# Optimization experiments

Hardware: AMD Instinct MI355X
Metric: run time of the kernel (lower is better)

## Reference

```python
import jax, jax.numpy as jnp
import numpy as np

EMBED, H1, H2, IMG, MID, VOCAB = 1024, 1024, 1024, 2048, 512, 32000
N_REGIONS = 576


def lstm_cell(x, h, c, W_ih, W_hh, b_ih, b_hh):
    # PyTorch LSTM gate order: i, f, g, o
    g = x @ W_ih.T + b_ih + h @ W_hh.T + b_hh
    i, f, gg, o = jnp.split(g, 4, axis=-1)
    i, f, o = jax.nn.sigmoid(i), jax.nn.sigmoid(f), jax.nn.sigmoid(o)
    c_new = f * c + i * jnp.tanh(gg)
    h_new = o * jnp.tanh(c_new)
    return h_new, c_new


def setup_inputs() -> dict:
    key = jax.random.key(0)
    ks = jax.random.split(key, 24)
    s = 0.02
    in1 = H2 + IMG + EMBED   # lstm1 input size = 4096
    in2 = H1 + IMG           # lstm2 input size = 3072
    return {
        "V": jax.random.normal(ks[0], (N_REGIONS, IMG), jnp.float32),
        "w": jax.random.randint(ks[1], (1,), 0, VOCAB),
        "h1": jax.random.normal(ks[2], (1, 1, H1), jnp.float32),
        "c1": jax.random.normal(ks[3], (1, 1, H1), jnp.float32),
        "h2": jax.random.normal(ks[4], (1, 1, H2), jnp.float32),
        "c2": jax.random.normal(ks[5], (1, 1, H2), jnp.float32),
        "emb": jax.random.normal(ks[6], (VOCAB, EMBED), jnp.float32) * s,
        "W_ih1": jax.random.normal(ks[7], (4 * H1, in1), jnp.float32) * s,
        "W_hh1": jax.random.normal(ks[8], (4 * H1, H1), jnp.float32) * s,
        "b_ih1": jax.random.normal(ks[9], (4 * H1,), jnp.float32) * s,
        "b_hh1": jax.random.normal(ks[10], (4 * H1,), jnp.float32) * s,
        "W_ih2": jax.random.normal(ks[11], (4 * H2, in2), jnp.float32) * s,
        "W_hh2": jax.random.normal(ks[12], (4 * H2, H2), jnp.float32) * s,
        "b_ih2": jax.random.normal(ks[13], (4 * H2,), jnp.float32) * s,
        "b_hh2": jax.random.normal(ks[14], (4 * H2,), jnp.float32) * s,
        "lv_w": jax.random.normal(ks[15], (MID, IMG), jnp.float32) * s,
        "lv_b": jax.random.normal(ks[16], (MID,), jnp.float32) * s,
        "lh_w": jax.random.normal(ks[17], (MID, H1), jnp.float32) * s,
        "lh_b": jax.random.normal(ks[18], (MID,), jnp.float32) * s,
        "att_w": jax.random.normal(ks[19], (1, MID), jnp.float32) * s,
        "att_b": jax.random.normal(ks[20], (1,), jnp.float32) * s,
        "lin_w": jax.random.normal(ks[21], (VOCAB, H2), jnp.float32) * s,
        "lin_b": jax.random.normal(ks[22], (VOCAB,), jnp.float32) * s,
    }


def reference(V, w, h1, c1, h2, c2, emb, W_ih1, W_hh1, b_ih1, b_hh1,
              W_ih2, W_hh2, b_ih2, b_hh2, lv_w, lv_b, lh_w, lh_b,
              att_w, att_b, lin_w, lin_b):
    vbar = V.mean(axis=0, keepdims=True)                 # [1, IMG]
    we = emb[w]                                          # [1, EMBED]
    x1 = jnp.concatenate([h2[0], vbar, we], axis=1)      # [1, H2+IMG+EMBED]
    h1n, c1n = lstm_cell(x1, h1[0], c1[0], W_ih1, W_hh1, b_ih1, b_hh1)

    vt = V @ lv_w.T + lv_b                               # [N, MID]
    h1t = h1n @ lh_w.T + lh_b                            # [1, MID] (broadcast = repeat)
    a = jnp.tanh(vt + h1t) @ att_w.T + att_b             # [N, 1]
    a = jax.nn.softmax(a, axis=0)                        # softmax over regions
    v = (a * V).sum(axis=0, keepdims=True)               # [1, IMG]

    x2 = jnp.concatenate([v, h1n], axis=1)               # [1, H1+IMG]
    h2n, c2n = lstm_cell(x2, h2[0], c2[0], W_ih2, W_hh2, b_ih2, b_hh2)

    o = h2n @ lin_w.T + lin_b                            # [1, VOCAB]
    return (o, h1n[None], c1n[None], h2n[None], c2n[None])
```

## Files before the change

### kernel.cpp

```cpp
#include <hip/hip_runtime.h>

#define H     1024
#define IMG   2048
#define MID   512
#define VOCAB 32000
#define NR    576
#define IN1   4096
#define IN2   3072
#define VN    (NR * IMG)
#define WN    (MID * IMG)

typedef unsigned short u16;
typedef unsigned int u32;
typedef __attribute__((ext_vector_type(8))) short short8;
typedef __attribute__((ext_vector_type(4))) float f32x4;

__device__ __forceinline__ float wave_sum(float v) {
  #pragma unroll
  for (int off = 32; off > 0; off >>= 1) v += __shfl_down(v, off, 64);
  return v;
}
__device__ __forceinline__ float sigf(float x) { return 1.0f / (1.0f + __expf(-x)); }
__device__ __forceinline__ float dot4(float4 a, float4 b) {
  return a.x * b.x + a.y * b.y + a.z * b.z + a.w * b.w;
}
__device__ __forceinline__ u32 f2bfbits(float f) {
  union { float f; u32 i; } c; c.f = f;
  return (c.i + 0x7fffu + ((c.i >> 16) & 1u)) >> 16;
}

__global__ __launch_bounds__(256) void k_prep(const float* __restrict__ V,
                                              const float* __restrict__ lvw,
                                              const float* __restrict__ h2,
                                              const float* __restrict__ emb,
                                              const int* __restrict__ w,
                                              u16* __restrict__ Vbf, u16* __restrict__ Wbf,
                                              float* __restrict__ x1) {
  int b = blockIdx.x;
  int t = threadIdx.x;
  if (b < 1088) {
    long i8 = (long)(b * 256 + t) * 8;
    const float* src; u16* dst; long off;
    if (i8 < VN) { src = V; dst = Vbf; off = i8; }
    else         { src = lvw; dst = Wbf; off = i8 - VN; }
    float4 qa = *(const float4*)(src + off);
    float4 qb = *(const float4*)(src + off + 4);
    u32 p0 = f2bfbits(qa.x) | (f2bfbits(qa.y) << 16);
    u32 p1 = f2bfbits(qa.z) | (f2bfbits(qa.w) << 16);
    u32 p2 = f2bfbits(qb.x) | (f2bfbits(qb.y) << 16);
    u32 p3 = f2bfbits(qb.z) | (f2bfbits(qb.w) << 16);
    *(uint4*)(dst + off) = make_uint4(p0, p1, p2, p3);
  } else if (b < 1096) {
    int tt = (b - 1088) * 256 + t;
    if (tt < H) x1[tt] = h2[tt];
    else {
      int j = tt - H;
      x1[3072 + j] = emb[(long)w[0] * 1024 + j];
    }
  } else {
    __shared__ float red[8][32];
    int bb = b - 1096;
    int c = bb * 32 + (t & 31);
    int rc = t >> 5;
    float s = 0.f;
    for (int r = rc * 72; r < rc * 72 + 72; r++) s += V[(long)r * IMG + c];
    red[rc][t & 31] = s;
    __syncthreads();
    if (t < 32) {
      float tot = 0.f;
      #pragma unroll
      for (int j = 0; j < 8; j++) tot += red[j][t];
      x1[H + bb * 32 + t] = tot * (1.0f / 576.0f);
    }
  }
}

__global__ __launch_bounds__(256) void k_vt_mfma(const u16* __restrict__ Vbf,
                                                 const u16* __restrict__ Wbf,
                                                 float* __restrict__ vtp) {
  int t = threadIdx.x;
  int wave = t >> 6, lane = t & 63;
  int wm = wave >> 1, wn = wave & 1;
  int m0 = blockIdx.x * 64 + wm * 32;
  int n0 = blockIdx.y * 64 + wn * 32;
  int z  = blockIdx.z;
  int ri = lane & 15, quad = lane >> 4;
  const u16* aptr0 = Vbf + (long)(m0 + ri) * IMG + z * 512 + quad * 8;
  const u16* aptr1 = aptr0 + 16 * IMG;
  const u16* bptr0 = Wbf + (long)(n0 + ri) * IMG + z * 512 + quad * 8;
  const u16* bptr1 = bptr0 + 16 * IMG;
  f32x4 acc00 = {0.f,0.f,0.f,0.f}, acc01 = {0.f,0.f,0.f,0.f};
  f32x4 acc10 = {0.f,0.f,0.f,0.f}, acc11 = {0.f,0.f,0.f,0.f};
  #pragma unroll 4
  for (int ks = 0; ks < 16; ks++) {
    int ko = ks * 32;
    short8 a0 = *(const short8*)(aptr0 + ko);
    short8 a1 = *(const short8*)(aptr1 + ko);
    short8 b0 = *(const short8*)(bptr0 + ko);
    short8 b1 = *(const short8*)(bptr1 + ko);
    acc00 = __builtin_amdgcn_mfma_f32_16x16x32_bf16(a0, b0, acc00, 0, 0, 0);
    acc01 = __builtin_amdgcn_mfma_f32_16x16x32_bf16(a0, b1, acc01, 0, 0, 0);
    acc10 = __builtin_amdgcn_mfma_f32_16x16x32_bf16(a1, b0, acc10, 0, 0, 0);
    acc11 = __builtin_amdgcn_mfma_f32_16x16x32_bf16(a1, b1, acc11, 0, 0, 0);
  }
  float* base = vtp + (long)z * (NR * MID);
  #pragma unroll
  for (int r = 0; r < 4; r++) {
    int row = quad * 4 + r;
    base[(long)(m0 + row) * MID + n0 + ri]           = acc00[r];
    base[(long)(m0 + row) * MID + n0 + 16 + ri]      = acc01[r];
    base[(long)(m0 + 16 + row) * MID + n0 + ri]      = acc10[r];
    base[(long)(m0 + 16 + row) * MID + n0 + 16 + ri] = acc11[r];
  }
}

__global__ __launch_bounds__(256) void k_lstm1(const float* __restrict__ Wih,
                                               const float* __restrict__ Whh,
                                               const float* __restrict__ bih,
                                               const float* __restrict__ bhh,
                                               const float* __restrict__ x1,
                                               const float* __restrict__ h1,
                                               const float* __restrict__ c1,
                                               float* __restrict__ h1n,
                                               float* __restrict__ out_h,
                                               float* __restrict__ out_c) {
  __shared__ float gate[4];
  int w = threadIdx.x >> 6, l = threadIdx.x & 63;
  int k = blockIdx.x;
  int row = k + w * H;
  const float4* W4  = (const float4*)(Wih + (long)row * IN1);
  const float4* Wh4 = (const float4*)(Whh + (long)row * H);
  const float4* X4  = (const float4*)x1;
  const float4* H14 = (const float4*)h1;
  float acc = 0.f;
  #pragma unroll
  for (int c = 0; c < 16; c++) { int idx = c * 64 + l; acc += dot4(W4[idx], X4[idx]); }
  #pragma unroll
  for (int c = 0; c < 4; c++)  { int idx = c * 64 + l; acc += dot4(Wh4[idx], H14[idx]); }
  acc = wave_sum(acc);
  if (l == 0) gate[w] = acc + bih[row] + bhh[row];
  __syncthreads();
  if (threadIdx.x == 0) {
    float i  = sigf(gate[0]);
    float f  = sigf(gate[1]);
    float gg = tanhf(gate[2]);
    float o  = sigf(gate[3]);
    float c  = f * c1[k] + i * gg;
    float h  = o * tanhf(c);
    h1n[k] = h; out_h[k] = h; out_c[k] = c;
  }
}

__global__ void k_h1t(const float* __restrict__ lhw, const float* __restrict__ lhb,
                      const float* __restrict__ h1n, float* __restrict__ h1t) {
  int w = threadIdx.x >> 6, l = threadIdx.x & 63;
  int row = blockIdx.x * 4 + w;
  const float4* W4 = (const float4*)(lhw + (long)row * H);
  const float4* X4 = (const float4*)h1n;
  float acc = 0.f;
  #pragma unroll
  for (int c = 0; c < 4; c++) { int idx = c * 64 + l; acc += dot4(W4[idx], X4[idx]); }
  acc = wave_sum(acc);
  if (l == 0) h1t[row] = acc + lhb[row];
}

__global__ void k_att(const float* __restrict__ vtp, const float* __restrict__ lvb,
                      const float* __restrict__ h1t,
                      const float* __restrict__ attw, const float* __restrict__ attb,
                      float* __restrict__ logits) {
  int w = threadIdx.x >> 6, l = threadIdx.x & 63;
  int row = blockIdx.x * 4 + w;
  const float4* A4 = (const float4*)attw;
  const float4* T4 = (const float4*)h1t;
  const float4* B4 = (const float4*)lvb;
  float acc = 0.f;
  #pragma unroll
  for (int ch = 0; ch < 2; ch++) {
    int idx = 2 * l + ch;
    const float4* p = (const float4*)(vtp + (long)row * MID) + idx;
    float4 s = p[0];
    float4 s1 = p[NR * MID / 4];
    float4 s2 = p[2 * NR * MID / 4];
    float4 s3 = p[3 * NR * MID / 4];
    float4 bb = B4[idx], tt = T4[idx], aa = A4[idx];
    float vx = s.x + s1.x + s2.x + s3.x + bb.x + tt.x;
    float vy = s.y + s1.y + s2.y + s3.y + bb.y + tt.y;
    float vz = s.z + s1.z + s2.z + s3.z + bb.z + tt.z;
    float vw = s.w + s1.w + s2.w + s3.w + bb.w + tt.w;
    acc += tanhf(vx) * aa.x + tanhf(vy) * aa.y + tanhf(vz) * aa.z + tanhf(vw) * aa.w;
  }
  acc = wave_sum(acc);
  if (l == 0) logits[row] = acc + attb[0];
}

__global__ __launch_bounds__(256) void k_smwv(const float* __restrict__ logits,
                                              const float* __restrict__ V,
                                              float* __restrict__ v) {
  __shared__ float arr[576];
  __shared__ float red[8];
  int t = threadIdx.x;
  int wv = t >> 6, l = t & 63;
  float x0 = logits[t];
  float x1 = logits[t + 256];
  float x2 = (t < 64) ? logits[t + 512] : -3.0e38f;
  float m = fmaxf(fmaxf(x0, x1), x2);
  #pragma unroll
  for (int off = 32; off > 0; off >>= 1) m = fmaxf(m, __shfl_down(m, off, 64));
  if (l == 0) red[wv] = m;
  __syncthreads();
  float bm = fmaxf(fmaxf(red[0], red[1]), fmaxf(red[2], red[3]));
  float e0 = __expf(x0 - bm);
  float e1 = __expf(x1 - bm);
  float e2 = (t < 64) ? __expf(x2 - bm) : 0.f;
  arr[t] = e0; arr[t + 256] = e1;
  if (t < 64) arr[t + 512] = e2;
  float s = wave_sum(e0 + e1 + e2);
  __syncthreads();
  if (l == 0) red[4 + wv] = s;
  __syncthreads();
  float bsum = red[4] + red[5] + red[6] + red[7];
  float inv = 1.0f / bsum;
  int c = blockIdx.x * 256 + t;
  float acc = 0.f;
  #pragma unroll 8
  for (int r = 0; r < NR; r++) acc += arr[r] * V[(long)r * IMG + c];
  v[c] = acc * inv;
}

__global__ __launch_bounds__(256) void k_lstm2(const float* __restrict__ Wih,
                                               const float* __restrict__ Whh,
                                               const float* __restrict__ bih,
                                               const float* __restrict__ bhh,
                                               const float* __restrict__ v,
                                               const float* __restrict__ h1n,
                                               const float* __restrict__ h2,
                                               const float* __restrict__ c2,
                                               float* __restrict__ h2n,
                                               float* __restrict__ out_h,
                                               float* __restrict__ out_c) {
  __shared__ float gate[4];
  int w = threadIdx.x >> 6, l = threadIdx.x & 63;
  int k = blockIdx.x;
  int row = k + w * H;
  const float4* W4  = (const float4*)(Wih + (long)row * IN2);
  const float4* Wh4 = (const float4*)(Whh + (long)row * H);
  const float4* Vv4 = (const float4*)v;
  const float4* H1n = (const float4*)h1n;
  const float4* H24 = (const float4*)h2;
  float acc = 0.f;
  #pragma unroll
  for (int c = 0; c < 8; c++) { int idx = c * 64 + l; acc += dot4(W4[idx], Vv4[idx]); }
  #pragma unroll
  for (int c = 0; c < 4; c++) { int idx = c * 64 + l; acc += dot4(W4[512 + idx], H1n[idx]); }
  #pragma unroll
  for (int c = 0; c < 4; c++) { int idx = c * 64 + l; acc += dot4(Wh4[idx], H24[idx]); }
  acc = wave_sum(acc);
  if (l == 0) gate[w] = acc + bih[row] + bhh[row];
  __syncthreads();
  if (threadIdx.x == 0) {
    float i  = sigf(gate[0]);
    float f  = sigf(gate[1]);
    float gg = tanhf(gate[2]);
    float o  = sigf(gate[3]);
    float c  = f * c2[k] + i * gg;
    float h  = o * tanhf(c);
    h2n[k] = h; out_h[k] = h; out_c[k] = c;
  }
}

__global__ void k_out(const float* __restrict__ linw, const float* __restrict__ linb,
                      const float* __restrict__ h2n, float* __restrict__ o) {
  int w = threadIdx.x >> 6, l = threadIdx.x & 63;
  int row = blockIdx.x * 4 + w;
  const float4* W4 = (const float4*)(linw + (long)row * H);
  const float4* X4 = (const float4*)h2n;
  float acc = 0.f;
  #pragma unroll
  for (int c = 0; c < 4; c++) { int idx = c * 64 + l; acc += dot4(W4[idx], X4[idx]); }
  acc = wave_sum(acc);
  if (l == 0) o[row] = acc + linb[row];
}

extern "C" void kernel_launch(void* const* d_in, const int* in_sizes, int n_in,
                              void* d_out, int out_size, void* d_ws, size_t ws_size,
                              hipStream_t stream) {
  const float* V    = (const float*)d_in[0];
  const int*   w    = (const int*)d_in[1];
  const float* h1   = (const float*)d_in[2];
  const float* c1   = (const float*)d_in[3];
  const float* h2   = (const float*)d_in[4];
  const float* c2   = (const float*)d_in[5];
  const float* emb  = (const float*)d_in[6];
  const float* Wih1 = (const float*)d_in[7];
  const float* Whh1 = (const float*)d_in[8];
  const float* bih1 = (const float*)d_in[9];
  const float* bhh1 = (const float*)d_in[10];
  const float* Wih2 = (const float*)d_in[11];
  const float* Whh2 = (const float*)d_in[12];
  const float* bih2 = (const float*)d_in[13];
  const float* bhh2 = (const float*)d_in[14];
  const float* lvw  = (const float*)d_in[15];
  const float* lvb  = (const float*)d_in[16];
  const float* lhw  = (const float*)d_in[17];
  const float* lhb  = (const float*)d_in[18];
  const float* attw = (const float*)d_in[19];
  const float* attb = (const float*)d_in[20];
  const float* linw = (const float*)d_in[21];
  const float* linb = (const float*)d_in[22];

  float* ws     = (float*)d_ws;
  float* x1     = ws;
  float* h1n    = ws + 4096;
  float* h1t    = ws + 5120;
  float* logits = ws + 5632;
  float* v      = ws + 6272;
  float* h2n    = ws + 8320;
  float* vtp    = ws + 9344;
  u16*   Vbf    = (u16*)(ws + 1188992);
  u16*   Wbf    = Vbf + VN;

  float* out    = (float*)d_out;
  float* out_o  = out;
  float* out_h1 = out + VOCAB;
  float* out_c1 = out + VOCAB + H;
  float* out_h2 = out + VOCAB + 2 * H;
  float* out_c2 = out + VOCAB + 3 * H;

  k_prep<<<1160, 256, 0, stream>>>(V, lvw, h2, emb, w, Vbf, Wbf, x1);
  k_vt_mfma<<<dim3(9, 8, 4), 256, 0, stream>>>(Vbf, Wbf, vtp);
  k_lstm1<<<1024, 256, 0, stream>>>(Wih1, Whh1, bih1, bhh1, x1, h1, c1, h1n, out_h1, out_c1);
  k_h1t<<<128, 256, 0, stream>>>(lhw, lhb, h1n, h1t);
  k_att<<<144, 256, 0, stream>>>(vtp, lvb, h1t, attw, attb, logits);
  k_smwv<<<8, 256, 0, stream>>>(logits, V, v);
  k_lstm2<<<1024, 256, 0, stream>>>(Wih2, Whh2, bih2, bhh2, v, h1n, h2, c2, h2n, out_h2, out_c2);
  k_out<<<8000, 256, 0, stream>>>(linw, linb, h2n, out_o);
}
```

Baseline: 432.6 us.

## Merge vt GEMM with LSTM1 launch and widen softmax-weighted sum grid

The independent vt MFMA GEMM and the first LSTM cell now run as one launch, with block-index ranges picking the role, so both can occupy the GPU at once and one launch is saved. The softmax-weighted sum over V moves from 8 blocks to 64 blocks. Each block now covers 32 columns, with 8 row-chunks reduced through shared memory, which adds parallelism to a kernel that is bandwidth-bound and had far too few blocks. Mixing two kinds of block in one grid makes occupancy and register use depend on the heavier path.

```diff
diff --git a/kernel.cpp b/kernel.cpp
--- a/kernel.cpp
+++ b/kernel.cpp
@@ -75,79 +75,82 @@
   }
 }
 
-__global__ __launch_bounds__(256) void k_vt_mfma(const u16* __restrict__ Vbf,
-                                                 const u16* __restrict__ Wbf,
-                                                 float* __restrict__ vtp) {
+__global__ __launch_bounds__(256) void k_gemm_lstm1(const u16* __restrict__ Vbf,
+                                                    const u16* __restrict__ Wbf,
+                                                    float* __restrict__ vtp,
+                                                    const float* __restrict__ Wih,
+                                                    const float* __restrict__ Whh,
+                                                    const float* __restrict__ bih,
+                                                    const float* __restrict__ bhh,
+                                                    const float* __restrict__ x1,
+                                                    const float* __restrict__ h1,
+                                                    const float* __restrict__ c1,
+                                                    float* __restrict__ h1n,
+                                                    float* __restrict__ out_h,
+                                                    float* __restrict__ out_c) {
   int t = threadIdx.x;
-  int wave = t >> 6, lane = t & 63;
-  int wm = wave >> 1, wn = wave & 1;
-  int m0 = blockIdx.x * 64 + wm * 32;
-  int n0 = blockIdx.y * 64 + wn * 32;
-  int z  = blockIdx.z;
-  int ri = lane & 15, quad = lane >> 4;
-  const u16* aptr0 = Vbf + (long)(m0 + ri) * IMG + z * 512 + quad * 8;
-  const u16* aptr1 = aptr0 + 16 * IMG;
-  const u16* bptr0 = Wbf + (long)(n0 + ri) * IMG + z * 512 + quad * 8;
-  const u16* bptr1 = bptr0 + 16 * IMG;
-  f32x4 acc00 = {0.f,0.f,0.f,0.f}, acc01 = {0.f,0.f,0.f,0.f};
-  f32x4 acc10 = {0.f,0.f,0.f,0.f}, acc11 = {0.f,0.f,0.f,0.f};
-  #pragma unroll 4
-  for (int ks = 0; ks < 16; ks++) {
-    int ko = ks * 32;
-    short8 a0 = *(const short8*)(aptr0 + ko);
-    short8 a1 = *(const short8*)(aptr1 + ko);
-    short8 b0 = *(const short8*)(bptr0 + ko);
-    short8 b1 = *(const short8*)(bptr1 + ko);
-    acc00 = __builtin_amdgcn_mfma_f32_16x16x32_bf16(a0, b0, acc00, 0, 0, 0);
-    acc01 = __builtin_amdgcn_mfma_f32_16x16x32_bf16(a0, b1, acc01, 0, 0, 0);
-    acc10 = __builtin_amdgcn_mfma_f32_16x16x32_bf16(a1, b0, acc10, 0, 0, 0);
-    acc11 = __builtin_amdgcn_mfma_f32_16x16x32_bf16(a1, b1, acc11, 0, 0, 0);
-  }
-  float* base = vtp + (long)z * (NR * MID);
-  #pragma unroll
-  for (int r = 0; r < 4; r++) {
-    int row = quad * 4 + r;
-    base[(long)(m0 + row) * MID + n0 + ri]           = acc00[r];
-    base[(long)(m0 + row) * MID + n0 + 16 + ri]      = acc01[r];
-    base[(long)(m0 + 16 + row) * MID + n0 + ri]      = acc10[r];
-    base[(long)(m0 + 16 + row) * MID + n0 + 16 + ri] = acc11[r];
-  }
-}
-
-__global__ __launch_bounds__(256) void k_lstm1(const float* __restrict__ Wih,
-                                               const float* __restrict__ Whh,
-                                               const float* __restrict__ bih,
-                                               const float* __restrict__ bhh,
-                                               const float* __restrict__ x1,
-                                               const float* __restrict__ h1,
-                                               const float* __restrict__ c1,
-                                               float* __restrict__ h1n,
-                                               float* __restrict__ out_h,
-                                               float* __restrict__ out_c) {
-  __shared__ float gate[4];
-  int w = threadIdx.x >> 6, l = threadIdx.x & 63;
-  int k = blockIdx.x;
-  int row = k + w * H;
-  const float4* W4  = (const float4*)(Wih + (long)row * IN1);
-  const float4* Wh4 = (const float4*)(Whh + (long)row * H);
-  const float4* X4  = (const float4*)x1;
-  const float4* H14 = (const float4*)h1;
-  float acc = 0.f;
-  #pragma unroll
-  for (int c = 0; c < 16; c++) { int idx = c * 64 + l; acc += dot4(W4[idx], X4[idx]); }
-  #pragma unroll
-  for (int c = 0; c < 4; c++)  { int idx = c * 64 + l; acc += dot4(Wh4[idx], H14[idx]); }
-  acc = wave_sum(acc);
-  if (l == 0) gate[w] = acc + bih[row] + bhh[row];
-  __syncthreads();
-  if (threadIdx.x == 0) {
-    float i  = sigf(gate[0]);
-    float f  = sigf(gate[1]);
-    float gg = tanhf(gate[2]);
-    float o  = sigf(gate[3]);
-    float c  = f * c1[k] + i * gg;
-    float h  = o * tanhf(c);
-    h1n[k] = h; out_h[k] = h; out_c[k] = c;
+  int b = blockIdx.x;
+  if (b < 288) {
+    int z = b / 72, rem = b % 72;
+    int bx = rem % 9, by = rem / 9;
+    int wave = t >> 6, lane = t & 63;
+    int wm = wave >> 1, wn = wave & 1;
+    int m0 = bx * 64 + wm * 32;
+    int n0 = by * 64 + wn * 32;
+    int ri = lane & 15, quad = lane >> 4;
+    const u16* aptr0 = Vbf + (long)(m0 + ri) * IMG + z * 512 + quad * 8;
+    const u16* aptr1 = aptr0 + 16 * IMG;
+    const u16* bptr0 = Wbf + (long)(n0 + ri) * IMG + z * 512 + quad * 8;
+    const u16* bptr1 = bptr0 + 16 * IMG;
+    f32x4 acc00 = {0.f,0.f,0.f,0.f}, acc01 = {0.f,0.f,0.f,0.f};
+    f32x4 acc10 = {0.f,0.f,0.f,0.f}, acc11 = {0.f,0.f,0.f,0.f};
+    #pragma unroll 4
+    for (int ks = 0; ks < 16; ks++) {
+      int ko = ks * 32;
+      short8 a0 = *(const short8*)(aptr0 + ko);
+      short8 a1 = *(const short8*)(aptr1 + ko);
+      short8 b0 = *(const short8*)(bptr0 + ko);
+      short8 b1 = *(const short8*)(bptr1 + ko);
+      acc00 = __builtin_amdgcn_mfma_f32_16x16x32_bf16(a0, b0, acc00, 0, 0, 0);
+      acc01 = __builtin_amdgcn_mfma_f32_16x16x32_bf16(a0, b1, acc01, 0, 0, 0);
+      acc10 = __builtin_amdgcn_mfma_f32_16x16x32_bf16(a1, b0, acc10, 0, 0, 0);
+      acc11 = __builtin_amdgcn_mfma_f32_16x16x32_bf16(a1, b1, acc11, 0, 0, 0);
+    }
+    float* base = vtp + (long)z * (NR * MID);
+    #pragma unroll
+    for (int r = 0; r < 4; r++) {
+      int row = quad * 4 + r;
+      base[(long)(m0 + row) * MID + n0 + ri]           = acc00[r];
+      base[(long)(m0 + row) * MID + n0 + 16 + ri]      = acc01[r];
+      base[(long)(m0 + 16 + row) * MID + n0 + ri]      = acc10[r];
+      base[(long)(m0 + 16 + row) * MID + n0 + 16 + ri] = acc11[r];
+    }
+  } else {
+    __shared__ float gate[4];
+    int w = t >> 6, l = t & 63;
+    int k = b - 288;
+    int row = k + w * H;
+    const float4* W4  = (const float4*)(Wih + (long)row * IN1);
+    const float4* Wh4 = (const float4*)(Whh + (long)row * H);
+    const float4* X4  = (const float4*)x1;
+    const float4* H14 = (const float4*)h1;
+    float acc = 0.f;
+    #pragma unroll
+    for (int c = 0; c < 16; c++) { int idx = c * 64 + l; acc += dot4(W4[idx], X4[idx]); }
+    #pragma unroll
+    for (int c = 0; c < 4; c++)  { int idx = c * 64 + l; acc += dot4(Wh4[idx], H14[idx]); }
+    acc = wave_sum(acc);
+    if (l == 0) gate[w] = acc + bih[row] + bhh[row];
+    __syncthreads();
+    if (t == 0) {
+      float i  = sigf(gate[0]);
+      float f  = sigf(gate[1]);
+      float gg = tanhf(gate[2]);
+      float o  = sigf(gate[3]);
+      float c  = f * c1[k] + i * gg;
+      float h  = o * tanhf(c);
+      h1n[k] = h; out_h[k] = h; out_c[k] = c;
+    }
   }
 }
 
@@ -197,7 +200,8 @@
                                               const float* __restrict__ V,
                                               float* __restrict__ v) {
   __shared__ float arr[576];
-  __shared__ float red[8];
+  __shared__ float r8[8];
+  __shared__ float red[8][32];
   int t = threadIdx.x;
   int wv = t >> 6, l = t & 63;
   float x0 = logits[t];
@@ -206,25 +210,31 @@
   float m = fmaxf(fmaxf(x0, x1), x2);
   #pragma unroll
   for (int off = 32; off > 0; off >>= 1) m = fmaxf(m, __shfl_down(m, off, 64));
-  if (l == 0) red[wv] = m;
+  if (l == 0) r8[wv] = m;
   __syncthreads();
-  float bm = fmaxf(fmaxf(red[0], red[1]), fmaxf(red[2], red[3]));
+  float bm = fmaxf(fmaxf(r8[0], r8[1]), fmaxf(r8[2], r8[3]));
   float e0 = __expf(x0 - bm);
   float e1 = __expf(x1 - bm);
   float e2 = (t < 64) ? __expf(x2 - bm) : 0.f;
   arr[t] = e0; arr[t + 256] = e1;
   if (t < 64) arr[t + 512] = e2;
   float s = wave_sum(e0 + e1 + e2);
+  if (l == 0) r8[4 + wv] = s;
   __syncthreads();
-  if (l == 0) red[4 + wv] = s;
+  float inv = 1.0f / (r8[4] + r8[5] + r8[6] + r8[7]);
+  int c = blockIdx.x * 32 + (t & 31);
+  int rc = t >> 5;
+  float acc = 0.f;
+  #pragma unroll 8
+  for (int r = rc * 72; r < rc * 72 + 72; r++) acc += arr[r] * V[(long)r * IMG + c];
+  red[rc][t & 31] = acc;
   __syncthreads();
-  float bsum = red[4] + red[5] + red[6] + red[7];
-  float inv = 1.0f / bsum;
-  int c = blockIdx.x * 256 + t;
-  float acc = 0.f;
-  #pragma unroll 8
-  for (int r = 0; r < NR; r++) acc += arr[r] * V[(long)r * IMG + c];
-  v[c] = acc * inv;
+  if (t < 32) {
+    float tot = 0.f;
+    #pragma unroll
+    for (int j = 0; j < 8; j++) tot += red[j][t];
+    v[blockIdx.x * 32 + t] = tot * inv;
+  }
 }
 
 __global__ __launch_bounds__(256) void k_lstm2(const float* __restrict__ Wih,
@@ -327,11 +337,11 @@
   float* out_c2 = out + VOCAB + 3 * H;
 
   k_prep<<<1160, 256, 0, stream>>>(V, lvw, h2, emb, w, Vbf, Wbf, x1);
-  k_vt_mfma<<<dim3(9, 8, 4), 256, 0, stream>>>(Vbf, Wbf, vtp);
-  k_lstm1<<<1024, 256, 0, stream>>>(Wih1, Whh1, bih1, bhh1, x1, h1, c1, h1n, out_h1, out_c1);
+  k_gemm_lstm1<<<1312, 256, 0, stream>>>(Vbf, Wbf, vtp, Wih1, Whh1, bih1, bhh1,
+                                         x1, h1, c1, h1n, out_h1, out_c1);
   k_h1t<<<128, 256, 0, stream>>>(lhw, lhb, h1n, h1t);
   k_att<<<144, 256, 0, stream>>>(vtp, lvb, h1t, attw, attb, logits);
-  k_smwv<<<8, 256, 0, stream>>>(logits, V, v);
+  k_smwv<<<64, 256, 0, stream>>>(logits, V, v);
   k_lstm2<<<1024, 256, 0, stream>>>(Wih2, Whh2, bih2, bhh2, v, h1n, h2, c2, h2n, out_h2, out_c2);
   k_out<<<8000, 256, 0, stream>>>(linw, linb, h2n, out_o);
 }
```

After: 401.5 us. -7.2%, faster.
